# Kernel tuning notes

Measured on AMD Instinct MI355X. Metric: run time of the kernel, lower is better.

Reference implementation:

```python
import jax, jax.numpy as jnp
import numpy as np

B, N, D = 32, 32768, 128

def setup_inputs() -> dict:
    key = jax.random.key(0)
    k1, k2, k3 = jax.random.split(key, 3)
    inputs = jax.random.normal(k1, (B, D), dtype=jnp.float32)
    # alphas must be in (0,1): variance = 1 - alpha
    alphas = jax.random.uniform(k2, (B,), dtype=jnp.float32, minval=0.05, maxval=0.95)
    data_batch = jax.random.normal(k3, (N, D), dtype=jnp.float32)
    return {"inputs": inputs, "alphas": alphas, "data_batch": data_batch}

def reference(inputs, alphas, data_batch):
    # inputs: [B, D], alphas: [B], data_batch: [N, D]
    d = inputs.shape[-1]
    sqrt_a = jnp.sqrt(alphas)[:, None]          # [B, 1]
    var = (1.0 - alphas)[:, None]                # [B, 1]
    # means = sqrt(alpha) * data -> [B, N, D]; squared distance summed over D
    diff = inputs[:, None, :] - sqrt_a[:, :, None] * data_batch[None]  # [B, N, D]
    sq = jnp.sum(diff * diff, axis=-1)           # [B, N]
    # logits summed over feature dim: -(0.5*D*log(var) + 0.5/var * sq)
    logits = -(0.5 * d * jnp.log(var) + 0.5 / var * sq)  # [B, N]
    probs = jax.nn.softmax(logits, axis=1)       # [B, N]
    x0 = probs @ data_batch                      # [B, D]
    return (inputs - sqrt_a * x0) / jnp.sqrt(var)
```

## Files before the change

kernel.cpp:

```cpp
#include <hip/hip_runtime.h>
#include <math.h>

#define BB 32
#define DD 128
#define NN 32768

#define NB 512
#define RPB 64
#define WS_STRIDE 136
#define NP NB

typedef __attribute__((ext_vector_type(8))) short bf16x8;
typedef __attribute__((ext_vector_type(4))) float f32x4;

#define O_RH   0
#define O_RL   16384
#define O_INH  32768
#define O_INL  40960
#define O_RT   49152
#define O_D1   65536
#define O_NRM  75776
#define O_PT   O_INH
#define O_X0   O_RH
#define ARENA  76032

__device__ __forceinline__ unsigned bf16_rne(float x) {
    unsigned u = __builtin_bit_cast(unsigned, x);
    return (u + 0x7FFFu + ((u >> 16) & 1u)) >> 16;
}
__device__ __forceinline__ float bf16f(unsigned h) {
    return __builtin_bit_cast(float, h << 16);
}
__device__ __forceinline__ unsigned pk2(float a, float b) {
    return bf16_rne(a) | (bf16_rne(b) << 16);
}

__global__ __launch_bounds__(256) void bayes_k1(
    const float* __restrict__ inputs, const float* __restrict__ alphas,
    const float* __restrict__ data, float* __restrict__ ws)
{
    __shared__ __align__(16) char arena[ARENA];

    const int tid  = threadIdx.x;
    const int lane = tid & 63;
    const int wv   = tid >> 6;
    const int ln   = lane & 15;
    const int g    = lane >> 4;
    const int bid  = blockIdx.x;

    {
        const int r = tid >> 2, c4 = tid & 3;
        const float4* gp = (const float4*)(data + ((size_t)bid * RPB + r) * DD + c4 * 32);
        float v[32];
        #pragma unroll
        for (int i = 0; i < 8; ++i) {
            const float4 t4 = gp[i];
            v[4*i+0] = t4.x; v[4*i+1] = t4.y; v[4*i+2] = t4.z; v[4*i+3] = t4.w;
        }
        float nn = 0.0f;
        #pragma unroll
        for (int i = 0; i < 32; ++i) nn = fmaf(v[i], v[i], nn);
        nn += __shfl_xor(nn, 1);
        nn += __shfl_xor(nn, 2);
        if (c4 == 0) *(float*)(arena + O_NRM + r * 4) = nn;

        const int swz = (r & 7) << 4;
        #pragma unroll
        for (int u = 0; u < 4; ++u) {
            unsigned hw[4], lw[4];
            #pragma unroll
            for (int j = 0; j < 4; ++j) {
                const float a = v[u*8 + 2*j], b = v[u*8 + 2*j + 1];
                const unsigned ah = bf16_rne(a), bh = bf16_rne(b);
                hw[j] = ah | (bh << 16);
                lw[j] = pk2(a - bf16f(ah), b - bf16f(bh));
            }
            const int go = (c4 * 64 + u * 16) ^ swz;
            *(uint4*)(arena + O_RH + r * 256 + go) = make_uint4(hw[0], hw[1], hw[2], hw[3]);
            *(uint4*)(arena + O_RL + r * 256 + go) = make_uint4(lw[0], lw[1], lw[2], lw[3]);
        }
    }

    {
        const int b = tid >> 3, c8 = tid & 7;
        const float4* gp = (const float4*)(inputs + b * DD + c8 * 16);
        float v[16];
        #pragma unroll
        for (int i = 0; i < 4; ++i) {
            const float4 t4 = gp[i];
            v[4*i+0] = t4.x; v[4*i+1] = t4.y; v[4*i+2] = t4.z; v[4*i+3] = t4.w;
        }
        const int swz = (b & 7) << 4;
        #pragma unroll
        for (int u = 0; u < 2; ++u) {
            unsigned hw[4], lw[4];
            #pragma unroll
            for (int j = 0; j < 4; ++j) {
                const float a = v[u*8 + 2*j], bb = v[u*8 + 2*j + 1];
                const unsigned ah = bf16_rne(a), bh = bf16_rne(bb);
                hw[j] = ah | (bh << 16);
                lw[j] = pk2(a - bf16f(ah), bb - bf16f(bh));
            }
            const int go = (c8 * 32 + u * 16) ^ swz;
            *(uint4*)(arena + O_INH + b * 256 + go) = make_uint4(hw[0], hw[1], hw[2], hw[3]);
            *(uint4*)(arena + O_INL + b * 256 + go) = make_uint4(lw[0], lw[1], lw[2], lw[3]);
        }
    }

    {
        const int d = tid >> 1, rh = tid & 1;
        const float* gc = data + ((size_t)bid * RPB + rh * 32) * DD + d;
        const int swz = (d & 7) << 4;
        #pragma unroll
        for (int u = 0; u < 4; ++u) {
            unsigned w[4];
            #pragma unroll
            for (int j = 0; j < 4; ++j)
                w[j] = pk2(gc[(u*8 + 2*j) * DD], gc[(u*8 + 2*j + 1) * DD]);
            *(uint4*)(arena + O_RT + d * 128 + ((rh * 64 + u * 16) ^ swz)) =
                make_uint4(w[0], w[1], w[2], w[3]);
        }
    }
    __syncthreads();

    const int ni = wv & 1;
    const int kh = wv >> 1;
    f32x4 acc1[4];
    #pragma unroll
    for (int mt = 0; mt < 4; ++mt)
        #pragma unroll
        for (int i = 0; i < 4; ++i) acc1[mt][i] = 0.0f;

    #pragma unroll
    for (int ks = 0; ks < 2; ++ks) {
        const int kbyte = kh * 128 + ks * 64 + g * 16;
        const int n = ni * 16 + ln;
        const bf16x8 Bh = *(const bf16x8*)(arena + O_INH + n * 256 + (kbyte ^ ((n & 7) << 4)));
        const bf16x8 Bl = *(const bf16x8*)(arena + O_INL + n * 256 + (kbyte ^ ((n & 7) << 4)));
        #pragma unroll
        for (int mt = 0; mt < 4; ++mt) {
            const int r = mt * 16 + ln;
            const bf16x8 Ah = *(const bf16x8*)(arena + O_RH + r * 256 + (kbyte ^ ((r & 7) << 4)));
            const bf16x8 Al = *(const bf16x8*)(arena + O_RL + r * 256 + (kbyte ^ ((r & 7) << 4)));
            acc1[mt] = __builtin_amdgcn_mfma_f32_16x16x32_bf16(Ah, Bh, acc1[mt], 0, 0, 0);
            acc1[mt] = __builtin_amdgcn_mfma_f32_16x16x32_bf16(Al, Bh, acc1[mt], 0, 0, 0);
            acc1[mt] = __builtin_amdgcn_mfma_f32_16x16x32_bf16(Ah, Bl, acc1[mt], 0, 0, 0);
        }
    }
    if (kh == 1) {
        #pragma unroll
        for (int mt = 0; mt < 4; ++mt)
            *(f32x4*)(arena + O_D1 + ((ni * 4 + mt) * 16 + ln) * 80 + g * 16) = acc1[mt];
    }
    __syncthreads();

    if (kh == 0) {
        const int b = ni * 16 + ln;
        #pragma unroll
        for (int mt = 0; mt < 4; ++mt) {
            const f32x4 o = *(const f32x4*)(arena + O_D1 + ((ni * 4 + mt) * 16 + ln) * 80 + g * 16);
            #pragma unroll
            for (int i = 0; i < 4; ++i) acc1[mt][i] += o[i];
        }
        const float alpha = alphas[b];
        const float var = 1.0f - alpha;
        const float c1 = sqrtf(alpha) / var;
        const float c2 = 0.5f * alpha / var;

        float lg[4][4];
        float mx = -1e30f;
        #pragma unroll
        for (int mt = 0; mt < 4; ++mt) {
            const f32x4 nr4 = *(const f32x4*)(arena + O_NRM + (mt * 16 + g * 4) * 4);
            #pragma unroll
            for (int i = 0; i < 4; ++i) {
                lg[mt][i] = fmaf(c1, acc1[mt][i], -c2 * nr4[i]);
                mx = fmaxf(mx, lg[mt][i]);
            }
        }
        mx = fmaxf(mx, __shfl_xor(mx, 16));
        mx = fmaxf(mx, __shfl_xor(mx, 32));

        float ss = 0.0f;
        const int swz = (b & 7) << 4;
        #pragma unroll
        for (int mt = 0; mt < 4; ++mt) {
            float e0 = __expf(lg[mt][0] - mx), e1 = __expf(lg[mt][1] - mx);
            float e2 = __expf(lg[mt][2] - mx), e3 = __expf(lg[mt][3] - mx);
            ss += (e0 + e1) + (e2 + e3);
            *(uint2*)(arena + O_PT + b * 128 + ((mt * 32 + g * 8) ^ swz)) =
                make_uint2(pk2(e0, e1), pk2(e2, e3));
        }
        ss += __shfl_xor(ss, 16);
        ss += __shfl_xor(ss, 32);
        if (g == 0) {
            float* wsp = ws + ((size_t)b * NB + bid) * WS_STRIDE;
            wsp[0] = mx; wsp[1] = ss;
        }
    }
    __syncthreads();

    {
        f32x4 acc2[2][2];
        #pragma unroll
        for (int a = 0; a < 2; ++a)
            #pragma unroll
            for (int c = 0; c < 2; ++c)
                #pragma unroll
                for (int i = 0; i < 4; ++i) acc2[a][c][i] = 0.0f;

        #pragma unroll
        for (int ks = 0; ks < 2; ++ks) {
            bf16x8 Bp[2];
            #pragma unroll
            for (int nt = 0; nt < 2; ++nt) {
                const int b2 = nt * 16 + ln;
                Bp[nt] = *(const bf16x8*)(arena + O_PT + b2 * 128 +
                                          ((ks * 64 + g * 16) ^ ((b2 & 7) << 4)));
            }
            #pragma unroll
            for (int mt2 = 0; mt2 < 2; ++mt2) {
                const int d = wv * 32 + mt2 * 16 + ln;
                const bf16x8 Ar = *(const bf16x8*)(arena + O_RT + d * 128 +
                                                   ((ks * 64 + g * 16) ^ ((d & 7) << 4)));
                #pragma unroll
                for (int nt = 0; nt < 2; ++nt)
                    acc2[mt2][nt] = __builtin_amdgcn_mfma_f32_16x16x32_bf16(Ar, Bp[nt], acc2[mt2][nt], 0, 0, 0);
            }
        }
        #pragma unroll
        for (int mt2 = 0; mt2 < 2; ++mt2)
            #pragma unroll
            for (int nt = 0; nt < 2; ++nt) {
                const int b = nt * 16 + ln;
                const int d0 = wv * 32 + mt2 * 16 + g * 4;
                *(f32x4*)(arena + O_X0 + b * 512 + ((d0 * 4) ^ ((b & 7) << 4))) = acc2[mt2][nt];
            }
    }
    __syncthreads();

    {
        const int b = tid >> 3, c8 = tid & 7;
        const int swz = (b & 7) << 4;
        float* dst = ws + ((size_t)b * NB + bid) * WS_STRIDE + 4 + c8 * 16;
        #pragma unroll
        for (int u = 0; u < 4; ++u) {
            const f32x4 v = *(const f32x4*)(arena + O_X0 + b * 512 + ((c8 * 64 + u * 16) ^ swz));
            *(f32x4*)(dst + u * 4) = v;
        }
    }
}

__global__ __launch_bounds__(256) void bayes_k2(
    const float* __restrict__ inputs, const float* __restrict__ alphas,
    const float* __restrict__ ws, float* __restrict__ out)
{
    const int b   = blockIdx.x >> 2;
    const int dq  = blockIdx.x & 3;
    const int tid = threadIdx.x;

    __shared__ float e_s[NP];
    __shared__ float red_s[16];
    __shared__ float part[8][32];

    const float* base_b = ws + (size_t)b * NP * WS_STRIDE;

    float mi[2], si[2];
    #pragma unroll
    for (int q = 0; q < 2; ++q) {
        const int i = tid + q * 256;
        mi[q] = base_b[(size_t)i * WS_STRIDE];
        si[q] = base_b[(size_t)i * WS_STRIDE + 1];
    }

    float mm = fmaxf(mi[0], mi[1]);
    #pragma unroll
    for (int off = 1; off <= 32; off <<= 1) mm = fmaxf(mm, __shfl_xor(mm, off));
    if ((tid & 63) == 0) red_s[tid >> 6] = mm;
    __syncthreads();
    const float M = fmaxf(fmaxf(red_s[0], red_s[1]), fmaxf(red_s[2], red_s[3]));

    float ss = 0.0f;
    #pragma unroll
    for (int q = 0; q < 2; ++q) {
        const float ei = __expf(mi[q] - M);
        e_s[tid + q * 256] = ei;
        ss = fmaf(si[q], ei, ss);
    }
    #pragma unroll
    for (int off = 1; off <= 32; off <<= 1) ss += __shfl_xor(ss, off);
    if ((tid & 63) == 0) red_s[8 + (tid >> 6)] = ss;
    __syncthreads();
    const float S = (red_s[8] + red_s[9]) + (red_s[10] + red_s[11]);

    const int dd = tid & 31, ii = tid >> 5;
    const int d  = dq * 32 + dd;
    float x = 0.0f;
    #pragma unroll 8
    for (int k = 0; k < 64; ++k) {
        const int i = ii + k * 8;
        x = fmaf(e_s[i], base_b[(size_t)i * WS_STRIDE + 4 + d], x);
    }
    part[ii][dd] = x;
    __syncthreads();

    if (tid < 32) {
        float x0 = 0.0f;
        #pragma unroll
        for (int p = 0; p < 8; ++p) x0 += part[p][tid];
        x0 /= S;
        const float alpha = alphas[b];
        const float sa  = sqrtf(alpha);
        const float var = 1.0f - alpha;
        const int dout  = dq * 32 + tid;
        out[b * DD + dout] = (inputs[b * DD + dout] - sa * x0) / sqrtf(var);
    }
}

extern "C" void kernel_launch(void* const* d_in, const int* in_sizes, int n_in,
                              void* d_out, int out_size, void* d_ws, size_t ws_size,
                              hipStream_t stream)
{
    const float* inputs = (const float*)d_in[0];
    const float* alphas = (const float*)d_in[1];
    const float* data   = (const float*)d_in[2];
    float* out = (float*)d_out;
    float* ws  = (float*)d_ws;

    bayes_k1<<<NB, 256, 0, stream>>>(inputs, alphas, data, ws);
    bayes_k2<<<BB * 4, 256, 0, stream>>>(inputs, alphas, ws, out);
}
```

Before: 83.28 us.

## Halve rows per block, split MFMA by output tile, separate max/sum workspace

Each block now handles 32 data rows instead of 64, doubling the grid to 1024 blocks and roughly shrinking shared memory from 76KB to 45KB. The intent is more blocks resident per CU and better load balance. The first GEMM is split so each wave computes one 16x16 output tile over the full K, which removes the cross-wave K-half reduction and its extra barrier. Logits are staged through a new LDS buffer, and the per-block max/sum pairs move to a separate contiguous workspace region so the second kernel can load them as float2. The trade-off is twice as many partial x0 vectors, so the second kernel reads and reduces more workspace data.

Result: slower. 92.49 us (+11.1%).

```diff
diff --git a/kernel.cpp b/kernel.cpp
--- a/kernel.cpp
+++ b/kernel.cpp
@@ -5,24 +5,24 @@
 #define DD 128
 #define NN 32768
 
-#define NB 512
-#define RPB 64
-#define WS_STRIDE 136
+#define NB 1024
+#define RPB 32
 #define NP NB
+#define WS_MS_OFF ((size_t)BB * NB * DD)
 
 typedef __attribute__((ext_vector_type(8))) short bf16x8;
 typedef __attribute__((ext_vector_type(4))) float f32x4;
 
 #define O_RH   0
-#define O_RL   16384
-#define O_INH  32768
-#define O_INL  40960
-#define O_RT   49152
-#define O_D1   65536
-#define O_NRM  75776
+#define O_RL   8192
+#define O_INH  16384
+#define O_INL  24576
+#define O_RT   32768
+#define O_NRM  40960
+#define O_LQ   41088
+#define ARENA  45184
 #define O_PT   O_INH
 #define O_X0   O_RH
-#define ARENA  76032
 
 __device__ __forceinline__ unsigned bf16_rne(float x) {
     unsigned u = __builtin_bit_cast(unsigned, x);
@@ -49,24 +49,25 @@
     const int bid  = blockIdx.x;
 
     {
-        const int r = tid >> 2, c4 = tid & 3;
-        const float4* gp = (const float4*)(data + ((size_t)bid * RPB + r) * DD + c4 * 32);
-        float v[32];
-        #pragma unroll
-        for (int i = 0; i < 8; ++i) {
+        const int r = tid >> 3, c8 = tid & 7;
+        const float4* gp = (const float4*)(data + ((size_t)bid * RPB + r) * DD + c8 * 16);
+        float v[16];
+        #pragma unroll
+        for (int i = 0; i < 4; ++i) {
             const float4 t4 = gp[i];
             v[4*i+0] = t4.x; v[4*i+1] = t4.y; v[4*i+2] = t4.z; v[4*i+3] = t4.w;
         }
         float nn = 0.0f;
         #pragma unroll
-        for (int i = 0; i < 32; ++i) nn = fmaf(v[i], v[i], nn);
+        for (int i = 0; i < 16; ++i) nn = fmaf(v[i], v[i], nn);
         nn += __shfl_xor(nn, 1);
         nn += __shfl_xor(nn, 2);
-        if (c4 == 0) *(float*)(arena + O_NRM + r * 4) = nn;
+        nn += __shfl_xor(nn, 4);
+        if (c8 == 0) *(float*)(arena + O_NRM + r * 4) = nn;
 
         const int swz = (r & 7) << 4;
         #pragma unroll
-        for (int u = 0; u < 4; ++u) {
+        for (int u = 0; u < 2; ++u) {
             unsigned hw[4], lw[4];
             #pragma unroll
             for (int j = 0; j < 4; ++j) {
@@ -75,7 +76,7 @@
                 hw[j] = ah | (bh << 16);
                 lw[j] = pk2(a - bf16f(ah), b - bf16f(bh));
             }
-            const int go = (c4 * 64 + u * 16) ^ swz;
+            const int go = (c8 * 32 + u * 16) ^ swz;
             *(uint4*)(arena + O_RH + r * 256 + go) = make_uint4(hw[0], hw[1], hw[2], hw[3]);
             *(uint4*)(arena + O_RL + r * 256 + go) = make_uint4(lw[0], lw[1], lw[2], lw[3]);
         }
@@ -109,94 +110,76 @@
 
     {
         const int d = tid >> 1, rh = tid & 1;
-        const float* gc = data + ((size_t)bid * RPB + rh * 32) * DD + d;
-        const int swz = (d & 7) << 4;
-        #pragma unroll
-        for (int u = 0; u < 4; ++u) {
+        const float* gc = data + ((size_t)bid * RPB + rh * 16) * DD + d;
+        const int swz = (d & 3) << 4;
+        #pragma unroll
+        for (int u = 0; u < 2; ++u) {
             unsigned w[4];
             #pragma unroll
             for (int j = 0; j < 4; ++j)
                 w[j] = pk2(gc[(u*8 + 2*j) * DD], gc[(u*8 + 2*j + 1) * DD]);
-            *(uint4*)(arena + O_RT + d * 128 + ((rh * 64 + u * 16) ^ swz)) =
+            *(uint4*)(arena + O_RT + d * 64 + ((rh * 32 + u * 16) ^ swz)) =
                 make_uint4(w[0], w[1], w[2], w[3]);
         }
     }
     __syncthreads();
 
-    const int ni = wv & 1;
-    const int kh = wv >> 1;
-    f32x4 acc1[4];
-    #pragma unroll
-    for (int mt = 0; mt < 4; ++mt)
-        #pragma unroll
-        for (int i = 0; i < 4; ++i) acc1[mt][i] = 0.0f;
-
-    #pragma unroll
-    for (int ks = 0; ks < 2; ++ks) {
-        const int kbyte = kh * 128 + ks * 64 + g * 16;
-        const int n = ni * 16 + ln;
-        const bf16x8 Bh = *(const bf16x8*)(arena + O_INH + n * 256 + (kbyte ^ ((n & 7) << 4)));
-        const bf16x8 Bl = *(const bf16x8*)(arena + O_INL + n * 256 + (kbyte ^ ((n & 7) << 4)));
-        #pragma unroll
-        for (int mt = 0; mt < 4; ++mt) {
-            const int r = mt * 16 + ln;
-            const bf16x8 Ah = *(const bf16x8*)(arena + O_RH + r * 256 + (kbyte ^ ((r & 7) << 4)));
-            const bf16x8 Al = *(const bf16x8*)(arena + O_RL + r * 256 + (kbyte ^ ((r & 7) << 4)));
-            acc1[mt] = __builtin_amdgcn_mfma_f32_16x16x32_bf16(Ah, Bh, acc1[mt], 0, 0, 0);
-            acc1[mt] = __builtin_amdgcn_mfma_f32_16x16x32_bf16(Al, Bh, acc1[mt], 0, 0, 0);
-            acc1[mt] = __builtin_amdgcn_mfma_f32_16x16x32_bf16(Ah, Bl, acc1[mt], 0, 0, 0);
-        }
-    }
-    if (kh == 1) {
-        #pragma unroll
-        for (int mt = 0; mt < 4; ++mt)
-            *(f32x4*)(arena + O_D1 + ((ni * 4 + mt) * 16 + ln) * 80 + g * 16) = acc1[mt];
-    }
-    __syncthreads();
-
-    if (kh == 0) {
-        const int b = ni * 16 + ln;
-        #pragma unroll
-        for (int mt = 0; mt < 4; ++mt) {
-            const f32x4 o = *(const f32x4*)(arena + O_D1 + ((ni * 4 + mt) * 16 + ln) * 80 + g * 16);
-            #pragma unroll
-            for (int i = 0; i < 4; ++i) acc1[mt][i] += o[i];
-        }
+    {
+        const int mt = wv >> 1, nt = wv & 1;
+        const int r  = mt * 16 + ln;
+        const int b2 = nt * 16 + ln;
+        f32x4 acc1;
+        #pragma unroll
+        for (int i = 0; i < 4; ++i) acc1[i] = 0.0f;
+
+        #pragma unroll
+        for (int ks = 0; ks < 4; ++ks) {
+            const int kbyte = ks * 64 + g * 16;
+            const bf16x8 Bh = *(const bf16x8*)(arena + O_INH + b2 * 256 + (kbyte ^ ((b2 & 7) << 4)));
+            const bf16x8 Bl = *(const bf16x8*)(arena + O_INL + b2 * 256 + (kbyte ^ ((b2 & 7) << 4)));
+            const bf16x8 Ah = *(const bf16x8*)(arena + O_RH  + r  * 256 + (kbyte ^ ((r  & 7) << 4)));
+            const bf16x8 Al = *(const bf16x8*)(arena + O_RL  + r  * 256 + (kbyte ^ ((r  & 7) << 4)));
+            acc1 = __builtin_amdgcn_mfma_f32_16x16x32_bf16(Ah, Bh, acc1, 0, 0, 0);
+            acc1 = __builtin_amdgcn_mfma_f32_16x16x32_bf16(Al, Bh, acc1, 0, 0, 0);
+            acc1 = __builtin_amdgcn_mfma_f32_16x16x32_bf16(Ah, Bl, acc1, 0, 0, 0);
+        }
+        #pragma unroll
+        for (int i = 0; i < 4; ++i)
+            *(float*)(arena + O_LQ + (((mt * 16 + g * 4 + i) * 32) + nt * 16 + ln) * 4) = acc1[i];
+    }
+    __syncthreads();
+
+    if (wv < 2) {
+        const int b = wv * 16 + ln;
         const float alpha = alphas[b];
         const float var = 1.0f - alpha;
         const float c1 = sqrtf(alpha) / var;
         const float c2 = 0.5f * alpha / var;
 
-        float lg[4][4];
+        float lg[8];
         float mx = -1e30f;
         #pragma unroll
-        for (int mt = 0; mt < 4; ++mt) {
-            const f32x4 nr4 = *(const f32x4*)(arena + O_NRM + (mt * 16 + g * 4) * 4);
-            #pragma unroll
-            for (int i = 0; i < 4; ++i) {
-                lg[mt][i] = fmaf(c1, acc1[mt][i], -c2 * nr4[i]);
-                mx = fmaxf(mx, lg[mt][i]);
-            }
+        for (int j = 0; j < 8; ++j) {
+            const int r = g * 8 + j;
+            const float L  = *(const float*)(arena + O_LQ + (r * 32 + b) * 4);
+            const float nr = *(const float*)(arena + O_NRM + r * 4);
+            lg[j] = fmaf(c1, L, -c2 * nr);
+            mx = fmaxf(mx, lg[j]);
         }
         mx = fmaxf(mx, __shfl_xor(mx, 16));
         mx = fmaxf(mx, __shfl_xor(mx, 32));
 
+        float e[8];
         float ss = 0.0f;
-        const int swz = (b & 7) << 4;
-        #pragma unroll
-        for (int mt = 0; mt < 4; ++mt) {
-            float e0 = __expf(lg[mt][0] - mx), e1 = __expf(lg[mt][1] - mx);
-            float e2 = __expf(lg[mt][2] - mx), e3 = __expf(lg[mt][3] - mx);
-            ss += (e0 + e1) + (e2 + e3);
-            *(uint2*)(arena + O_PT + b * 128 + ((mt * 32 + g * 8) ^ swz)) =
-                make_uint2(pk2(e0, e1), pk2(e2, e3));
-        }
+        #pragma unroll
+        for (int j = 0; j < 8; ++j) { e[j] = __expf(lg[j] - mx); ss += e[j]; }
         ss += __shfl_xor(ss, 16);
         ss += __shfl_xor(ss, 32);
-        if (g == 0) {
-            float* wsp = ws + ((size_t)b * NB + bid) * WS_STRIDE;
-            wsp[0] = mx; wsp[1] = ss;
-        }
+
+        *(uint4*)(arena + O_PT + b * 64 + ((g * 16) ^ ((b & 3) << 4))) =
+            make_uint4(pk2(e[0], e[1]), pk2(e[2], e[3]), pk2(e[4], e[5]), pk2(e[6], e[7]));
+        if (g == 0)
+            *(float2*)(ws + WS_MS_OFF + ((size_t)b * NB + bid) * 2) = make_float2(mx, ss);
     }
     __syncthreads();
 
@@ -209,32 +192,27 @@
                 #pragma unroll
                 for (int i = 0; i < 4; ++i) acc2[a][c][i] = 0.0f;
 
-        #pragma unroll
-        for (int ks = 0; ks < 2; ++ks) {
-            bf16x8 Bp[2];
+        bf16x8 Bp[2];
+        #pragma unroll
+        for (int nt = 0; nt < 2; ++nt) {
+            const int b2 = nt * 16 + ln;
+            Bp[nt] = *(const bf16x8*)(arena + O_PT + b2 * 64 + ((g * 16) ^ ((b2 & 3) << 4)));
+        }
+        #pragma unroll
+        for (int a = 0; a < 2; ++a) {
+            const int d = (wv * 2 + a) * 16 + ln;
+            const bf16x8 Ar = *(const bf16x8*)(arena + O_RT + d * 64 + ((g * 16) ^ ((d & 3) << 4)));
+            #pragma unroll
+            for (int nt = 0; nt < 2; ++nt)
+                acc2[a][nt] = __builtin_amdgcn_mfma_f32_16x16x32_bf16(Ar, Bp[nt], acc2[a][nt], 0, 0, 0);
+        }
+        #pragma unroll
+        for (int a = 0; a < 2; ++a)
             #pragma unroll
             for (int nt = 0; nt < 2; ++nt) {
-                const int b2 = nt * 16 + ln;
-                Bp[nt] = *(const bf16x8*)(arena + O_PT + b2 * 128 +
-                                          ((ks * 64 + g * 16) ^ ((b2 & 7) << 4)));
-            }
-            #pragma unroll
-            for (int mt2 = 0; mt2 < 2; ++mt2) {
-                const int d = wv * 32 + mt2 * 16 + ln;
-                const bf16x8 Ar = *(const bf16x8*)(arena + O_RT + d * 128 +
-                                                   ((ks * 64 + g * 16) ^ ((d & 7) << 4)));
-                #pragma unroll
-                for (int nt = 0; nt < 2; ++nt)
-                    acc2[mt2][nt] = __builtin_amdgcn_mfma_f32_16x16x32_bf16(Ar, Bp[nt], acc2[mt2][nt], 0, 0, 0);
-            }
-        }
-        #pragma unroll
-        for (int mt2 = 0; mt2 < 2; ++mt2)
-            #pragma unroll
-            for (int nt = 0; nt < 2; ++nt) {
-                const int b = nt * 16 + ln;
-                const int d0 = wv * 32 + mt2 * 16 + g * 4;
-                *(f32x4*)(arena + O_X0 + b * 512 + ((d0 * 4) ^ ((b & 7) << 4))) = acc2[mt2][nt];
+                const int b  = nt * 16 + ln;
+                const int d0 = (wv * 2 + a) * 16 + g * 4;
+                *(f32x4*)(arena + O_X0 + b * 512 + ((d0 * 4) ^ ((b & 7) << 4))) = acc2[a][nt];
             }
     }
     __syncthreads();
@@ -242,7 +220,7 @@
     {
         const int b = tid >> 3, c8 = tid & 7;
         const int swz = (b & 7) << 4;
-        float* dst = ws + ((size_t)b * NB + bid) * WS_STRIDE + 4 + c8 * 16;
+        float* dst = ws + ((size_t)b * NB + bid) * DD + c8 * 16;
         #pragma unroll
         for (int u = 0; u < 4; ++u) {
             const f32x4 v = *(const f32x4*)(arena + O_X0 + b * 512 + ((c8 * 64 + u * 16) ^ swz));
@@ -263,17 +241,15 @@
     __shared__ float red_s[16];
     __shared__ float part[8][32];
 
-    const float* base_b = ws + (size_t)b * NP * WS_STRIDE;
-
-    float mi[2], si[2];
+    const float* msb = ws + WS_MS_OFF + (size_t)b * NP * 2;
+    float mi[4], si[4];
     #pragma unroll
-    for (int q = 0; q < 2; ++q) {
-        const int i = tid + q * 256;
-        mi[q] = base_b[(size_t)i * WS_STRIDE];
-        si[q] = base_b[(size_t)i * WS_STRIDE + 1];
-    }
-
-    float mm = fmaxf(mi[0], mi[1]);
+    for (int q = 0; q < 4; ++q) {
+        const float2 v = *(const float2*)(msb + (tid + q * 256) * 2);
+        mi[q] = v.x; si[q] = v.y;
+    }
+
+    float mm = fmaxf(fmaxf(mi[0], mi[1]), fmaxf(mi[2], mi[3]));
     #pragma unroll
     for (int off = 1; off <= 32; off <<= 1) mm = fmaxf(mm, __shfl_xor(mm, off));
     if ((tid & 63) == 0) red_s[tid >> 6] = mm;
@@ -282,7 +258,7 @@
 
     float ss = 0.0f;
     #pragma unroll
-    for (int q = 0; q < 2; ++q) {
+    for (int q = 0; q < 4; ++q) {
         const float ei = __expf(mi[q] - M);
         e_s[tid + q * 256] = ei;
         ss = fmaf(si[q], ei, ss);
@@ -295,13 +271,15 @@
 
     const int dd = tid & 31, ii = tid >> 5;
     const int d  = dq * 32 + dd;
-    float x = 0.0f;
-    #pragma unroll 8
-    for (int k = 0; k < 64; ++k) {
-        const int i = ii + k * 8;
-        x = fmaf(e_s[i], base_b[(size_t)i * WS_STRIDE + 4 + d], x);
-    }
-    part[ii][dd] = x;
+    const float* xb = ws + (size_t)b * NP * DD + d;
+    float x0a = 0.0f, x0b = 0.0f;
+    #pragma unroll 4
+    for (int k = 0; k < 128; k += 2) {
+        const int i0 = ii + k * 8, i1 = ii + (k + 1) * 8;
+        x0a = fmaf(e_s[i0], xb[(size_t)i0 * DD], x0a);
+        x0b = fmaf(e_s[i1], xb[(size_t)i1 * DD], x0b);
+    }
+    part[ii][dd] = x0a + x0b;
     __syncthreads();
 
     if (tid < 32) {
```
